# Kernel optimization log

Hardware: AMD Instinct MI355X
Metric: run time of the kernel (lower is better)

## Reference

```python
import jax, jax.numpy as jnp
import numpy as np

EMBEDDING_DIM = 256
NUM_EMBEDDINGS = 2048
COMMITMENT_COST = 0.25


def setup_inputs() -> dict:
    key = jax.random.key(0)
    k1, k2 = jax.random.split(key)
    inputs = jax.random.normal(k1, (32, EMBEDDING_DIM, 32, 32), dtype=jnp.float32)
    # learned codebook buffer, shape (D, K) as in the torch module
    embedding = jax.random.normal(k2, (EMBEDDING_DIM, NUM_EMBEDDINGS), dtype=jnp.float32)
    return {"inputs": inputs, "embedding": embedding}


def reference(inputs, embedding):
    # Eval-mode forward of VectorQuantizerEMA (EMA buffer updates are
    # training-only side effects and do not affect the returned values).
    B, D, H, W = inputs.shape
    K = embedding.shape[1]
    x = inputs.astype(jnp.float32)
    # (B, D, H, W) -> (N, D), N = B*H*W, clamped as in the source
    flat = jnp.clip(jnp.transpose(x, (0, 2, 3, 1)).reshape(-1, D), -10.0, 10.0)
    # squared L2 distances to every codeword: (N, K)
    distances = (
        jnp.sum(flat * flat, axis=1, keepdims=True)
        + jnp.sum(embedding * embedding, axis=0, keepdims=True)
        - 2.0 * (flat @ embedding)
    )
    encoding_indices = jnp.argmin(distances, axis=1)  # (N,)
    # one-hot @ emb.T is just a gather of codebook columns
    q_flat = jnp.take(embedding.T, encoding_indices, axis=0)  # (N, D)
    quantized = jnp.transpose(q_flat.reshape(B, H, W, D), (0, 3, 1, 2))
    # VQ losses (computed against the un-clamped float inputs, as in torch)
    e_latent_loss = jnp.mean((jax.lax.stop_gradient(quantized) - x) ** 2)
    q_latent_loss = jnp.mean((quantized - jax.lax.stop_gradient(x)) ** 2)
    loss = q_latent_loss + COMMITMENT_COST * e_latent_loss
    # straight-through estimator
    quantized_st = inputs + jax.lax.stop_gradient(quantized - inputs)
    # perplexity from codeword usage (mean one-hot == normalized counts)
    n = encoding_indices.shape[0]
    avg_probs = jnp.zeros((K,), dtype=jnp.float32).at[encoding_indices].add(1.0) / n
    perplexity = jnp.exp(-jnp.sum(avg_probs * jnp.log(avg_probs + 1e-10)))
    return quantized_st, loss, perplexity, encoding_indices
```

## Files before the change

### kernel.cpp

```cpp
#include <hip/hip_runtime.h>
#include <hip/hip_bf16.h>
#include <math.h>

typedef unsigned int  uint;
typedef unsigned short ushort;

#define DD    256
#define KK    2048
#define HW    1024
#define NN    32768
#define NUMEL 8388608
#define STRIDEB (DD*HW)
#define NBLK_QL (NUMEL/1024)

#define WS_H2     0
#define WS_COUNTS 8192
#define WS_EBF    16512
#define WS_PV     2113664
#define WS_PI     2375808
#define WS_BPART  2637952

#define OUT_LOSS  8388608
#define OUT_PPL   8388609
#define OUT_IDX   8388610

typedef __attribute__((ext_vector_type(8))) short  short8;
typedef __attribute__((ext_vector_type(4))) float  float4v;

typedef __attribute__((address_space(1))) uint guint;
typedef __attribute__((address_space(3))) uint luint;

__device__ __forceinline__ ushort f2bf(float f) {
    uint u = __float_as_uint(f);
    return (ushort)((u + 0x7FFFu + ((u >> 16) & 1u)) >> 16);
}

__global__ __launch_bounds__(256) void prep_emb(const float* __restrict__ emb,
                                                ushort* __restrict__ ebf,
                                                float* __restrict__ h2) {
    int g  = blockIdx.x * 256 + threadIdx.x;
    int k  = g & (KK - 1);
    int dg = g >> 11;
    int d0 = dg * 8;
    int s    = dg >> 2;
    int quad = dg & 3;
    int ct   = k >> 4;
    int l    = quad * 16 + (k & 15);

    union { ushort us[8]; uint4 v; } hu, lu;
    float p2 = 0.f;
#pragma unroll
    for (int j = 0; j < 8; ++j) {
        float v = emb[(size_t)(d0 + j) * KK + k];
        p2 += v * v;
        ushort hb = f2bf(v);
        float  hf = __uint_as_float(((uint)hb) << 16);
        hu.us[j] = hb;
        lu.us[j] = f2bf(v - hf);
    }
    size_t hi_off = (size_t)(((ct * 8 + s) * 2 + 0) * 64 + l) * 8;
    size_t lo_off = (size_t)(((ct * 8 + s) * 2 + 1) * 64 + l) * 8;
    *(uint4*)(ebf + hi_off) = hu.v;
    *(uint4*)(ebf + lo_off) = lu.v;
    atomicAdd(&h2[k], 0.5f * p2);
}

__global__ __launch_bounds__(256, 2) void argmin_mfma(
    const float*  __restrict__ x,
    const ushort* __restrict__ ebf,
    const float*  __restrict__ h2,
    float* __restrict__ pv,
    int*   __restrict__ pi)
{
    __shared__ ushort sB[2][8192];
    __shared__ float  sH2[1024];

    const int tid  = threadIdx.x;
    const int w    = tid >> 6;
    const int lane = tid & 63;
    const int m    = lane & 15;
    const int quad = lane >> 4;

    const int rb = blockIdx.x >> 1;
    const int ch = blockIdx.x & 1;
    const int n0 = rb * 128 + w * 32;
    const int b  = n0 >> 10;
    const int hwb = n0 & 1023;
    const float* xb = x + (size_t)b * STRIDEB;
    const int cbase = ch * 1024;
    const int ctg0  = cbase >> 4;

    auto stage = [&](ushort* dst, int ctg) {
        const char* gs = (const char*)(ebf + (size_t)ctg * 8192) + tid * 16;
        char*       ls = (char*)dst + tid * 16;
#pragma unroll
        for (int i = 0; i < 4; ++i)
            __builtin_amdgcn_global_load_lds((guint*)(gs + i * 4096),
                                             (luint*)(ls + i * 4096),
                                             16, 0, 0);
    };

    stage(sB[0], ctg0);
    ((float4*)sH2)[tid] = ((const float4*)(h2 + cbase))[tid];

    short8 xh[2][8], xl[2][8];
#pragma unroll
    for (int st = 0; st < 2; ++st) {
        const int hw = hwb + st * 16 + m;
#pragma unroll
        for (int s = 0; s < 8; ++s) {
            const float* p = xb + (size_t)(s * 32 + quad * 8) * HW + hw;
            short8 hh, ll;
#pragma unroll
            for (int j = 0; j < 8; ++j) {
                float v = p[(size_t)j * HW];
                v = fminf(fmaxf(v, -10.f), 10.f);
                ushort hb = f2bf(v);
                float  hf = __uint_as_float(((uint)hb) << 16);
                hh[j] = (short)hb;
                ll[j] = (short)f2bf(v - hf);
            }
            xh[st][s] = hh;
            xl[st][s] = ll;
        }
    }

    float bv[2][4] = {{1e30f,1e30f,1e30f,1e30f},{1e30f,1e30f,1e30f,1e30f}};
    int   bi[2][4] = {{0,0,0,0},{0,0,0,0}};

    auto compute_tile = [&](const ushort* sbc, int ct) {
        float4v ahh0 = {0,0,0,0}, ahl0 = {0,0,0,0}, alh0 = {0,0,0,0};
        float4v ahh1 = {0,0,0,0}, ahl1 = {0,0,0,0}, alh1 = {0,0,0,0};
#pragma unroll
        for (int s = 0; s < 8; ++s) {
            short8 eh = *(const short8*)&sbc[(s * 2 + 0) * 512 + lane * 8];
            short8 el = *(const short8*)&sbc[(s * 2 + 1) * 512 + lane * 8];
            alh0 = __builtin_amdgcn_mfma_f32_16x16x32_bf16(xl[0][s], eh, alh0, 0, 0, 0);
            ahl0 = __builtin_amdgcn_mfma_f32_16x16x32_bf16(xh[0][s], el, ahl0, 0, 0, 0);
            ahh0 = __builtin_amdgcn_mfma_f32_16x16x32_bf16(xh[0][s], eh, ahh0, 0, 0, 0);
            alh1 = __builtin_amdgcn_mfma_f32_16x16x32_bf16(xl[1][s], eh, alh1, 0, 0, 0);
            ahl1 = __builtin_amdgcn_mfma_f32_16x16x32_bf16(xh[1][s], el, ahl1, 0, 0, 0);
            ahh1 = __builtin_amdgcn_mfma_f32_16x16x32_bf16(xh[1][s], eh, ahh1, 0, 0, 0);
        }
        const int c  = cbase + ct * 16 + m;
        const float hv = sH2[ct * 16 + m];
#pragma unroll
        for (int i = 0; i < 4; ++i) {
            float s0 = hv - (ahh0[i] + (ahl0[i] + alh0[i]));
            float s1 = hv - (ahh1[i] + (ahl1[i] + alh1[i]));
            if (s0 < bv[0][i]) { bv[0][i] = s0; bi[0][i] = c; }
            if (s1 < bv[1][i]) { bv[1][i] = s1; bi[1][i] = c; }
        }
    };

    __syncthreads();

    for (int ct = 0; ct < 64; ct += 2) {
        stage(sB[1], ctg0 + ct + 1);
        compute_tile(sB[0], ct);
        __syncthreads();
        stage(sB[0], (ct + 2 < 64) ? (ctg0 + ct + 2) : ctg0);
        compute_tile(sB[1], ct + 1);
        __syncthreads();
    }

#pragma unroll
    for (int st = 0; st < 2; ++st) {
#pragma unroll
        for (int i = 0; i < 4; ++i) {
            float v  = bv[st][i];
            int   ix = bi[st][i];
#pragma unroll
            for (int msk = 8; msk >= 1; msk >>= 1) {
                float ov = __shfl_xor(v, msk, 64);
                int   oi = __shfl_xor(ix, msk, 64);
                if (ov < v || (ov == v && oi < ix)) { v = ov; ix = oi; }
            }
            if (m == 0) {
                int n = n0 + st * 16 + quad * 4 + i;
                pv[n * 2 + ch] = v;
                pi[n * 2 + ch] = ix;
            }
        }
    }
}

__global__ __launch_bounds__(256) void quant_loss_kernel(
    const float* __restrict__ x,
    const float* __restrict__ emb,
    const float* __restrict__ pv,
    const int*   __restrict__ pi,
    float* __restrict__ out_idx_f,
    int*   __restrict__ counts,
    float* __restrict__ outq,
    float* __restrict__ bpart)
{
    __shared__ float red[4];
    size_t o4 = ((size_t)blockIdx.x * 256 + threadIdx.x) * 4;
    int b  = (int)(o4 >> 18);
    int d  = (int)((o4 >> 10) & 255);
    int n  = b * HW + (int)(o4 & 1023);

    const float4* pv4 = (const float4*)(pv + (size_t)n * 2);
    const int4*   pi4 = (const int4*)(pi + (size_t)n * 2);
    float4 pva = pv4[0], pvb = pv4[1];
    int4   pia = pi4[0], pib = pi4[1];
    int i0 = (pva.y < pva.x) ? pia.y : pia.x;
    int i1 = (pva.w < pva.z) ? pia.w : pia.z;
    int i2 = (pvb.y < pvb.x) ? pib.y : pib.x;
    int i3 = (pvb.w < pvb.z) ? pib.w : pib.z;
    i0 = min(max(i0, 0), KK - 1); i1 = min(max(i1, 0), KK - 1);
    i2 = min(max(i2, 0), KK - 1); i3 = min(max(i3, 0), KK - 1);

    if (d == 0) {
        float4 ixf = { (float)i0, (float)i1, (float)i2, (float)i3 };
        *(float4*)(out_idx_f + n) = ixf;
        atomicAdd(&counts[i0], 1);
        atomicAdd(&counts[i1], 1);
        atomicAdd(&counts[i2], 1);
        atomicAdd(&counts[i3], 1);
    }

    const float* er = emb + (size_t)d * KK;
    float4 q;
    q.x = er[i0]; q.y = er[i1]; q.z = er[i2]; q.w = er[i3];
    const float4 xv = *(const float4*)(x + o4);
    *(float4*)(outq + o4) = q;
    float ax = q.x - xv.x, ay = q.y - xv.y, az = q.z - xv.z, aw = q.w - xv.w;
    float s = ax * ax + ay * ay + az * az + aw * aw;
#pragma unroll
    for (int off = 32; off > 0; off >>= 1) s += __shfl_down(s, off, 64);
    if ((threadIdx.x & 63) == 0) red[threadIdx.x >> 6] = s;
    __syncthreads();
    if (threadIdx.x == 0)
        bpart[blockIdx.x] = red[0] + red[1] + red[2] + red[3];
}

__global__ __launch_bounds__(256) void finalize_kernel(
    const int* __restrict__ counts,
    const float* __restrict__ bpart,
    float* __restrict__ out)
{
    __shared__ float redp[4], redl[4];
    int tid = threadIdx.x;
    float s = 0.f;
    for (int k = tid; k < KK; k += 256) {
        float p = (float)counts[k] * (1.0f / (float)NN);
        s += p * logf(p + 1e-10f);
    }
    float ls = 0.f;
    for (int k = tid; k < NBLK_QL; k += 256) ls += bpart[k];
#pragma unroll
    for (int off = 32; off > 0; off >>= 1) {
        s  += __shfl_down(s, off, 64);
        ls += __shfl_down(ls, off, 64);
    }
    if ((tid & 63) == 0) { redp[tid >> 6] = s; redl[tid >> 6] = ls; }
    __syncthreads();
    if (tid == 0) {
        float tot = redp[0] + redp[1] + redp[2] + redp[3];
        float lsum = redl[0] + redl[1] + redl[2] + redl[3];
        out[OUT_PPL]  = expf(-tot);
        out[OUT_LOSS] = lsum * 1.25f / (float)NUMEL;
    }
}

extern "C" void kernel_launch(void* const* d_in, const int* in_sizes, int n_in,
                              void* d_out, int out_size, void* d_ws, size_t ws_size,
                              hipStream_t stream) {
    const float* x   = (const float*)d_in[0];
    const float* emb = (const float*)d_in[1];
    float* out = (float*)d_out;
    char*  ws  = (char*)d_ws;

    float*  h2     = (float*)(ws + WS_H2);
    int*    counts = (int*)(ws + WS_COUNTS);
    ushort* ebf    = (ushort*)(ws + WS_EBF);
    float*  pv     = (float*)(ws + WS_PV);
    int*    pi     = (int*)(ws + WS_PI);
    float*  bpart  = (float*)(ws + WS_BPART);

    hipMemsetAsync(ws, 0, 16384, stream);
    prep_emb<<<256, 256, 0, stream>>>(emb, ebf, h2);
    argmin_mfma<<<512, 256, 0, stream>>>(x, ebf, h2, pv, pi);
    quant_loss_kernel<<<NBLK_QL, 256, 0, stream>>>(x, emb, pv, pi,
                                                   out + OUT_IDX, counts, out, bpart);
    finalize_kernel<<<1, 256, 0, stream>>>(counts, bpart, out);
}
```

Baseline: 207.6 us.

## Derive loss from argmin distances and stage codebook rows in LDS for gather

The argmin kernel now accumulates each row's squared norm of the clamped input and stores the full distance (|x|^2 + 2*partial) per half, so the loss is the sum of minimum distances. This removes the 32 MB re-read of x in the quantize kernel. The quantize kernel now loads two codebook rows into shared memory and gathers from LDS instead of doing scattered global reads. The risk is that the loss is computed against clamped inputs and bf16-split dot products rather than the exact fp32 unclamped difference, which may differ slightly. The finalize kernel now reduces over pv, reading 32K pairs in a single block.

```diff
diff --git a/kernel.cpp b/kernel.cpp
--- a/kernel.cpp
+++ b/kernel.cpp
@@ -11,14 +11,12 @@
 #define NN    32768
 #define NUMEL 8388608
 #define STRIDEB (DD*HW)
-#define NBLK_QL (NUMEL/1024)
 
 #define WS_H2     0
 #define WS_COUNTS 8192
 #define WS_EBF    16512
 #define WS_PV     2113664
 #define WS_PI     2375808
-#define WS_BPART  2637952
 
 #define OUT_LOSS  8388608
 #define OUT_PPL   8388609
@@ -104,6 +102,7 @@
     ((float4*)sH2)[tid] = ((const float4*)(h2 + cbase))[tid];
 
     short8 xh[2][8], xl[2][8];
+    float xs2[2] = {0.f, 0.f};
 #pragma unroll
     for (int st = 0; st < 2; ++st) {
         const int hw = hwb + st * 16 + m;
@@ -115,6 +114,7 @@
             for (int j = 0; j < 8; ++j) {
                 float v = p[(size_t)j * HW];
                 v = fminf(fmaxf(v, -10.f), 10.f);
+                xs2[st] += v * v;
                 ushort hb = f2bf(v);
                 float  hf = __uint_as_float(((uint)hb) << 16);
                 hh[j] = (short)hb;
@@ -123,6 +123,11 @@
             xh[st][s] = hh;
             xl[st][s] = ll;
         }
+    }
+#pragma unroll
+    for (int st = 0; st < 2; ++st) {
+        xs2[st] += __shfl_xor(xs2[st], 16, 64);
+        xs2[st] += __shfl_xor(xs2[st], 32, 64);
     }
 
     float bv[2][4] = {{1e30f,1e30f,1e30f,1e30f},{1e30f,1e30f,1e30f,1e30f}};
@@ -176,80 +181,99 @@
                 int   oi = __shfl_xor(ix, msk, 64);
                 if (ov < v || (ov == v && oi < ix)) { v = ov; ix = oi; }
             }
+            float xr = __shfl(xs2[st], quad * 4 + i, 16);
             if (m == 0) {
                 int n = n0 + st * 16 + quad * 4 + i;
-                pv[n * 2 + ch] = v;
+                pv[n * 2 + ch] = xr + 2.0f * v;
                 pi[n * 2 + ch] = ix;
             }
         }
     }
 }
 
-__global__ __launch_bounds__(256) void quant_loss_kernel(
-    const float* __restrict__ x,
+__global__ __launch_bounds__(256) void quant_kernel(
     const float* __restrict__ emb,
     const float* __restrict__ pv,
     const int*   __restrict__ pi,
     float* __restrict__ out_idx_f,
     int*   __restrict__ counts,
-    float* __restrict__ outq,
-    float* __restrict__ bpart)
+    float* __restrict__ outq)
 {
-    __shared__ float red[4];
-    size_t o4 = ((size_t)blockIdx.x * 256 + threadIdx.x) * 4;
-    int b  = (int)(o4 >> 18);
-    int d  = (int)((o4 >> 10) & 255);
-    int n  = b * HW + (int)(o4 & 1023);
-
-    const float4* pv4 = (const float4*)(pv + (size_t)n * 2);
-    const int4*   pi4 = (const int4*)(pi + (size_t)n * 2);
-    float4 pva = pv4[0], pvb = pv4[1];
-    int4   pia = pi4[0], pib = pi4[1];
-    int i0 = (pva.y < pva.x) ? pia.y : pia.x;
-    int i1 = (pva.w < pva.z) ? pia.w : pia.z;
-    int i2 = (pvb.y < pvb.x) ? pib.y : pib.x;
-    int i3 = (pvb.w < pvb.z) ? pib.w : pib.z;
-    i0 = min(max(i0, 0), KK - 1); i1 = min(max(i1, 0), KK - 1);
-    i2 = min(max(i2, 0), KK - 1); i3 = min(max(i3, 0), KK - 1);
-
-    if (d == 0) {
-        float4 ixf = { (float)i0, (float)i1, (float)i2, (float)i3 };
-        *(float4*)(out_idx_f + n) = ixf;
-        atomicAdd(&counts[i0], 1);
-        atomicAdd(&counts[i1], 1);
-        atomicAdd(&counts[i2], 1);
-        atomicAdd(&counts[i3], 1);
-    }
-
-    const float* er = emb + (size_t)d * KK;
-    float4 q;
-    q.x = er[i0]; q.y = er[i1]; q.z = er[i2]; q.w = er[i3];
-    const float4 xv = *(const float4*)(x + o4);
-    *(float4*)(outq + o4) = q;
-    float ax = q.x - xv.x, ay = q.y - xv.y, az = q.z - xv.z, aw = q.w - xv.w;
-    float s = ax * ax + ay * ay + az * az + aw * aw;
-#pragma unroll
-    for (int off = 32; off > 0; off >>= 1) s += __shfl_down(s, off, 64);
-    if ((threadIdx.x & 63) == 0) red[threadIdx.x >> 6] = s;
+    __shared__ float sE[4096];
+    __shared__ int   sIdx[1024];
+
+    const int tid  = threadIdx.x;
+    const int bidx = blockIdx.x;
+    const int b    = bidx >> 7;
+    const int dp   = bidx & 127;
+    const int d0   = dp * 2;
+    const int nbase = b * HW;
+
+    {
+        const float4* src = (const float4*)(emb + (size_t)d0 * KK);
+        float4* dst = (float4*)sE;
+#pragma unroll
+        for (int i = 0; i < 4; ++i) dst[tid + i * 256] = src[tid + i * 256];
+    }
+    {
+        const int n = nbase + tid * 4;
+        const float4* pv4 = (const float4*)(pv + (size_t)n * 2);
+        const int4*   pi4 = (const int4*)(pi + (size_t)n * 2);
+        float4 pva = pv4[0], pvb = pv4[1];
+        int4   pia = pi4[0], pib = pi4[1];
+        int i0 = (pva.y < pva.x) ? pia.y : pia.x;
+        int i1 = (pva.w < pva.z) ? pia.w : pia.z;
+        int i2 = (pvb.y < pvb.x) ? pib.y : pib.x;
+        int i3 = (pvb.w < pvb.z) ? pib.w : pib.z;
+        i0 = min(max(i0, 0), KK - 1); i1 = min(max(i1, 0), KK - 1);
+        i2 = min(max(i2, 0), KK - 1); i3 = min(max(i3, 0), KK - 1);
+        sIdx[tid * 4 + 0] = i0; sIdx[tid * 4 + 1] = i1;
+        sIdx[tid * 4 + 2] = i2; sIdx[tid * 4 + 3] = i3;
+        if (d0 == 0) {
+            float4 ixf = { (float)i0, (float)i1, (float)i2, (float)i3 };
+            *(float4*)(out_idx_f + n) = ixf;
+            atomicAdd(&counts[i0], 1);
+            atomicAdd(&counts[i1], 1);
+            atomicAdd(&counts[i2], 1);
+            atomicAdd(&counts[i3], 1);
+        }
+    }
     __syncthreads();
-    if (threadIdx.x == 0)
-        bpart[blockIdx.x] = red[0] + red[1] + red[2] + red[3];
-}
-
-__global__ __launch_bounds__(256) void finalize_kernel(
+
+    {
+        const int e   = tid * 8;
+        const int dl  = e >> 10;
+        const int hw0 = e & 1023;
+        const float* row = sE + dl * 2048;
+        float q[8];
+#pragma unroll
+        for (int j = 0; j < 8; ++j) q[j] = row[sIdx[hw0 + j]];
+        float4 q0 = { q[0], q[1], q[2], q[3] };
+        float4 q1 = { q[4], q[5], q[6], q[7] };
+        float* dst = outq + (size_t)bidx * 2048 + e;
+        *(float4*)(dst + 0) = q0;
+        *(float4*)(dst + 4) = q1;
+    }
+}
+
+__global__ __launch_bounds__(1024) void finalize_kernel(
     const int* __restrict__ counts,
-    const float* __restrict__ bpart,
+    const float* __restrict__ pv,
     float* __restrict__ out)
 {
-    __shared__ float redp[4], redl[4];
+    __shared__ float redp[16], redl[16];
     int tid = threadIdx.x;
     float s = 0.f;
-    for (int k = tid; k < KK; k += 256) {
+#pragma unroll
+    for (int k = tid; k < KK; k += 1024) {
         float p = (float)counts[k] * (1.0f / (float)NN);
         s += p * logf(p + 1e-10f);
     }
     float ls = 0.f;
-    for (int k = tid; k < NBLK_QL; k += 256) ls += bpart[k];
+    for (int n = tid; n < NN; n += 1024) {
+        float2 pp = *(const float2*)(pv + (size_t)n * 2);
+        ls += fminf(pp.x, pp.y);
+    }
 #pragma unroll
     for (int off = 32; off > 0; off >>= 1) {
         s  += __shfl_down(s, off, 64);
@@ -258,8 +282,9 @@
     if ((tid & 63) == 0) { redp[tid >> 6] = s; redl[tid >> 6] = ls; }
     __syncthreads();
     if (tid == 0) {
-        float tot = redp[0] + redp[1] + redp[2] + redp[3];
-        float lsum = redl[0] + redl[1] + redl[2] + redl[3];
+        float tot = 0.f, lsum = 0.f;
+#pragma unroll
+        for (int i = 0; i < 16; ++i) { tot += redp[i]; lsum += redl[i]; }
         out[OUT_PPL]  = expf(-tot);
         out[OUT_LOSS] = lsum * 1.25f / (float)NUMEL;
     }
@@ -278,12 +303,11 @@
     ushort* ebf    = (ushort*)(ws + WS_EBF);
     float*  pv     = (float*)(ws + WS_PV);
     int*    pi     = (int*)(ws + WS_PI);
-    float*  bpart  = (float*)(ws + WS_BPART);
 
     hipMemsetAsync(ws, 0, 16384, stream);
     prep_emb<<<256, 256, 0, stream>>>(emb, ebf, h2);
     argmin_mfma<<<512, 256, 0, stream>>>(x, ebf, h2, pv, pi);
-    quant_loss_kernel<<<NBLK_QL, 256, 0, stream>>>(x, emb, pv, pi,
-                                                   out + OUT_IDX, counts, out, bpart);
-    finalize_kernel<<<1, 256, 0, stream>>>(counts, bpart, out);
-}
+    quant_kernel<<<4096, 256, 0, stream>>>(emb, pv, pi,
+                                           out + OUT_IDX, counts, out);
+    finalize_kernel<<<1, 1024, 0, stream>>>(counts, pv, out);
+}
```

After: 209.0 us. Within noise of the previous version (+0.7%).
